# Kernel optimization log

Hardware: AMD Instinct MI355X
Metric: run time of the kernel (lower is better)

The kernel has to match this reference:

```python
import jax, jax.numpy as jnp
import numpy as np

EMBED_DIM = 512
B, N = 8, 2048


def setup_inputs() -> dict:
    key = jax.random.key(0)
    ks = jax.random.split(key, 9)
    d = EMBED_DIM
    s = 1.0 / np.sqrt(d)
    return {
        "x": jax.random.normal(ks[0], (B, N, d), dtype=jnp.float32),
        "Wq": jax.random.uniform(ks[1], (d, d), jnp.float32, -s, s),
        "bq": jax.random.uniform(ks[2], (d,), jnp.float32, -s, s),
        "Wk": jax.random.uniform(ks[3], (d, d), jnp.float32, -s, s),
        "bk": jax.random.uniform(ks[4], (d,), jnp.float32, -s, s),
        "Wv": jax.random.uniform(ks[5], (d, d), jnp.float32, -s, s),
        "bv": jax.random.uniform(ks[6], (d,), jnp.float32, -s, s),
        "Wo": jax.random.uniform(ks[7], (d, d), jnp.float32, -s, s),
        "bo": jax.random.uniform(ks[8], (d,), jnp.float32, -s, s),
    }


def reference(x, Wq, bq, Wk, bk, Wv, bv, Wo, bo):
    d = x.shape[-1]
    scale = d ** (-0.5)
    q = x @ Wq + bq              # [B, N, D]
    k = x @ Wk + bk
    v = x @ Wv + bv
    attn = jnp.einsum('bnd,bmd->bnm', q, k) * scale  # [B, N, N]
    attn = jax.nn.softmax(attn, axis=-1)
    out = jnp.einsum('bnm,bmd->bnd', attn, v)
    return out @ Wo + bo
```

## Files before the change

kernel.cpp:

```cpp
#include <hip/hip_runtime.h>
#include <hip/hip_bf16.h>
#include <hip/hip_fp8.h>
#include <stdint.h>

typedef __bf16 bf16;
typedef __attribute__((ext_vector_type(8))) short short8;
typedef __attribute__((ext_vector_type(4))) float f32x4;
typedef __attribute__((ext_vector_type(4))) bf16 bf16x4;
typedef __attribute__((ext_vector_type(8))) int int8v;
typedef __attribute__((ext_vector_type(4))) int int4v;

#define DIM 512
#define NBATCH 8
#define SEQ 2048

__device__ __forceinline__ void gld_lds16(const void* g, void* l) {
    __builtin_amdgcn_global_load_lds(
        (const __attribute__((address_space(1))) void*)g,
        (__attribute__((address_space(3))) void*)l,
        16, 0, 0);
}

__device__ __forceinline__ unsigned char f32_to_e4m3(float v) {
#if __has_builtin(__builtin_amdgcn_cvt_pk_fp8_f32)
    return (unsigned char)(__builtin_amdgcn_cvt_pk_fp8_f32(v, v, 0, false) & 0xff);
#else
    return __hip_cvt_float_to_fp8(v, __HIP_SATFINITE, __HIP_E4M3);
#endif
}

template <int MODE, int SWIZ>
__global__ __launch_bounds__(256) void gemm_bt(
    const bf16* __restrict__ A, const bf16* __restrict__ Bt,
    void* __restrict__ Cv, const float* __restrict__ bias,
    int N, int K, long long sC, float alpha, int gx)
{
    __shared__ bf16 smem[32768];
    bf16* Asb = smem;
    bf16* Bsb = smem + 16384;

    int bx, by;
    {
        const unsigned g = blockIdx.x;
        const unsigned xcd = g & 7;
        const unsigned t = g >> 3;
        const unsigned per = (gridDim.x >> 3) / (unsigned)gx;
        by = xcd * per + t / (unsigned)gx;
        bx = t % (unsigned)gx;
    }

    const int tid  = threadIdx.x;
    const int lane = tid & 63;
    const int w    = tid >> 6;
    const int wr   = w >> 1;
    const int wc   = w & 1;
    const int lm   = lane & 15;
    const int lk   = lane >> 4;
    const int fs   = lm & 7;
    const int rq   = tid >> 3;
    const int pc   = tid & 7;
    const int scol = ((pc ^ (rq & 7)) * 8);

    const bf16* Ag = A + (size_t)(by * 128) * K;
    const bf16* Bg = Bt + (size_t)(bx * 128) * K;

    f32x4 acc[4][4];
#pragma unroll
    for (int i = 0; i < 4; ++i)
#pragma unroll
        for (int j = 0; j < 4; ++j)
            acc[i][j] = (f32x4){0.f, 0.f, 0.f, 0.f};

    auto stage = [&](int kb, int buf) {
#pragma unroll
        for (int t = 0; t < 4; ++t) {
            const int r = t * 32 + rq;
            gld_lds16(Ag + (size_t)r * K + kb + scol,
                      Asb + buf * 8192 + t * 2048 + tid * 8);
            gld_lds16(Bg + (size_t)r * K + kb + scol,
                      Bsb + buf * 8192 + t * 2048 + tid * 8);
        }
    };
    auto compute = [&](int buf) {
        const bf16* Ab = Asb + buf * 8192;
        const bf16* Bb = Bsb + buf * 8192;
#pragma unroll
        for (int s = 0; s < 2; ++s) {
            const int u = ((s * 4 + lk) ^ fs) * 8;
            short8 fa[4], fb[4];
#pragma unroll
            for (int i = 0; i < 4; ++i)
                fa[i] = *(const short8*)&Ab[(wr * 64 + i * 16 + lm) * 64 + u];
#pragma unroll
            for (int j = 0; j < 4; ++j)
                fb[j] = *(const short8*)&Bb[(wc * 64 + j * 16 + lm) * 64 + u];
#pragma unroll
            for (int i = 0; i < 4; ++i)
#pragma unroll
                for (int j = 0; j < 4; ++j)
                    acc[i][j] = __builtin_amdgcn_mfma_f32_16x16x32_bf16(
                        fa[i], fb[j], acc[i][j], 0, 0, 0);
        }
    };

    stage(0, 0);
    __syncthreads();
    const int E = K >> 6;
#pragma unroll 2
    for (int e = 0; e < E; ++e) {
        if (e + 1 < E) stage((e + 1) << 6, (e + 1) & 1);
        compute(e & 1);
        __syncthreads();
    }

    if (MODE == 2) {
        float* ft = (float*)smem;
        float* outp = (float*)Cv;
#pragma unroll
        for (int h = 0; h < 2; ++h) {
            if (wr == h) {
#pragma unroll
                for (int i = 0; i < 4; ++i)
#pragma unroll
                    for (int j = 0; j < 4; ++j) {
                        const int col = wc * 64 + j * 16 + lm;
                        const float bv = bias[bx * 128 + col];
#pragma unroll
                        for (int r = 0; r < 4; ++r)
                            ft[(i * 16 + lk * 4 + r) * 132 + col] =
                                acc[i][j][r] + bv;
                    }
            }
            __syncthreads();
            const int rr = tid >> 5, cc = (tid & 31) * 4;
#pragma unroll
            for (int p = 0; p < 8; ++p) {
                const int row = p * 8 + rr;
                *(float4*)&outp[(size_t)(by * 128 + h * 64 + row) * N +
                                bx * 128 + cc] = *(const float4*)&ft[row * 132 + cc];
            }
            __syncthreads();
        }
        return;
    }

#pragma unroll
    for (int i = 0; i < 4; ++i)
#pragma unroll
        for (int j = 0; j < 4; ++j) {
            const int col = bx * 128 + wc * 64 + j * 16 + lm;
            const float bv = bias[col];
#pragma unroll
            for (int r = 0; r < 4; ++r)
                acc[i][j][r] += bv;
        }

    const int sub  = (bx * 128) >> 9;
    const int col0 = (bx * 128) & 511;

    if (sub < 2) {
        uint8_t* d8 = (uint8_t*)Cv + (size_t)sub * 8388608;
        uint8_t* t8 = (uint8_t*)smem;
#pragma unroll
        for (int h = 0; h < 2; ++h) {
            if (wr == h) {
#pragma unroll
                for (int i = 0; i < 4; ++i)
#pragma unroll
                    for (int j = 0; j < 4; ++j)
#pragma unroll
                        for (int r = 0; r < 4; ++r)
                            t8[(i * 16 + lk * 4 + r) * 144 + wc * 64 + j * 16 + lm] =
                                f32_to_e4m3(32.0f * acc[i][j][r]);
            }
            __syncthreads();
            const int rr = tid >> 3, cc = (tid & 7) * 16;
#pragma unroll
            for (int p = 0; p < 2; ++p) {
                const int row = p * 32 + rr;
                const uint4 raw = *(const uint4*)&t8[row * 144 + cc];
                *(uint4*)&d8[(size_t)(by * 128 + h * 64 + row) * 512 + col0 + cc] =
                    raw;
            }
            __syncthreads();
        }
    } else {
        bf16* dst = (bf16*)((uint8_t*)Cv + 16777216);
#pragma unroll
        for (int h = 0; h < 2; ++h) {
            if (wr == h) {
#pragma unroll
                for (int i = 0; i < 4; ++i)
#pragma unroll
                    for (int j = 0; j < 4; ++j)
#pragma unroll
                        for (int r = 0; r < 4; ++r)
                            smem[(i * 16 + lk * 4 + r) * 136 + wc * 64 + j * 16 + lm] =
                                (bf16)acc[i][j][r];
            }
            __syncthreads();
            const int rr0 = tid >> 4, cc = (tid & 15) * 8;
#pragma unroll
            for (int p = 0; p < 4; ++p) {
                const int row = p * 16 + rr0;
                const uint4 raw = *(const uint4*)&smem[row * 136 + cc];
                *(uint4*)&dst[(size_t)(by * 128 + h * 64 + row) * 512 + col0 + cc] =
                    raw;
            }
            __syncthreads();
        }
    }
}

template <int MODE>
__global__ __launch_bounds__(256) void gemm_mx(
    const uint8_t* __restrict__ A, const uint8_t* __restrict__ Bt,
    void* __restrict__ Cv, float* __restrict__ rsum,
    int N, int K, long long sA, long long sB, long long sC, float alpha,
    int gx)
{
    __shared__ uint8_t smem[32768];
    uint8_t* As = smem;
    uint8_t* Bs = smem + 16384;

    int bx, by, bz;
    {
        const unsigned g = blockIdx.x;
        bz = g & 7;
        const unsigned r = g >> 3;
        bx = r % (unsigned)gx;
        by = r / (unsigned)gx;
    }

    const int tid  = threadIdx.x;
    const int lane = tid & 63;
    const int w    = tid >> 6;
    const int wr   = w >> 1;
    const int wc   = w & 1;
    const int lm   = lane & 15;
    const int lk   = lane >> 4;
    const int rq   = tid >> 3;
    const int pc   = tid & 7;
    const int ssrc = (pc ^ (rq & 7)) * 16;
    const int ca   = ((2 * lk) ^ (lm & 7)) * 16;
    const int cb   = ((2 * lk + 1) ^ (lm & 7)) * 16;

    const size_t z = bz;
    const uint8_t* Ag = A + z * (size_t)sA + (size_t)(by * 128) * K;
    const uint8_t* Bg = Bt + z * (size_t)sB + (size_t)(bx * 128) * K;

    f32x4 acc[4][4];
#pragma unroll
    for (int i = 0; i < 4; ++i)
#pragma unroll
        for (int j = 0; j < 4; ++j)
            acc[i][j] = (f32x4){0.f, 0.f, 0.f, 0.f};

    for (int kb = 0; kb < K; kb += 128) {
#pragma unroll
        for (int t = 0; t < 4; ++t) {
            const int r = t * 32 + rq;
            gld_lds16(Ag + (size_t)r * K + kb + ssrc, As + t * 4096 + tid * 16);
            gld_lds16(Bg + (size_t)r * K + kb + ssrc, Bs + t * 4096 + tid * 16);
        }
        __syncthreads();

        int8v fa[4];
#pragma unroll
        for (int i = 0; i < 4; ++i) {
            const uint8_t* rp = As + (wr * 64 + i * 16 + lm) * 128;
            const int4v lo = *(const int4v*)(rp + ca);
            const int4v hi = *(const int4v*)(rp + cb);
            fa[i] = (int8v){lo[0], lo[1], lo[2], lo[3], hi[0], hi[1], hi[2], hi[3]};
        }
#pragma unroll
        for (int j = 0; j < 4; ++j) {
            const uint8_t* rp = Bs + (wc * 64 + j * 16 + lm) * 128;
            const int4v lo = *(const int4v*)(rp + ca);
            const int4v hi = *(const int4v*)(rp + cb);
            const int8v fb = (int8v){lo[0], lo[1], lo[2], lo[3],
                                     hi[0], hi[1], hi[2], hi[3]};
#pragma unroll
            for (int i = 0; i < 4; ++i)
                acc[i][j] = __builtin_amdgcn_mfma_scale_f32_16x16x128_f8f6f4(
                    fa[i], fb, acc[i][j], 0, 0, 0, 127, 0, 127);
        }
        __syncthreads();
    }

    const int orow0 = by * 128 + wr * 64;

    if (MODE == 4) {
#pragma unroll
        for (int i = 0; i < 4; ++i) {
            float psum[4] = {0.f, 0.f, 0.f, 0.f};
#pragma unroll
            for (int j = 0; j < 4; ++j)
#pragma unroll
                for (int r = 0; r < 4; ++r) {
                    const float e = __expf(acc[i][j][r] * alpha);
                    acc[i][j][r] = e;
                    psum[r] += e;
                }
#pragma unroll
            for (int m = 1; m < 16; m <<= 1)
#pragma unroll
                for (int r = 0; r < 4; ++r) psum[r] += __shfl_xor(psum[r], m);
            if (lm == 0) {
#pragma unroll
                for (int r = 0; r < 4; ++r)
                    atomicAdd(&rsum[z * SEQ + orow0 + i * 16 + lk * 4 + r],
                              psum[r]);
            }
        }
        uint8_t* dst = (uint8_t*)Cv + z * (size_t)sC;
#pragma unroll
        for (int h = 0; h < 2; ++h) {
            if (wr == h) {
#pragma unroll
                for (int i = 0; i < 4; ++i)
#pragma unroll
                    for (int j = 0; j < 4; ++j)
#pragma unroll
                        for (int r = 0; r < 4; ++r)
                            smem[(i * 16 + lk * 4 + r) * 144 +
                                 wc * 64 + j * 16 + lm] =
                                f32_to_e4m3(acc[i][j][r]);
            }
            __syncthreads();
            const int rr = tid >> 3, cc = (tid & 7) * 16;
#pragma unroll
            for (int p = 0; p < 2; ++p) {
                const int row = p * 32 + rr;
                const uint4 raw = *(const uint4*)&smem[row * 144 + cc];
                *(uint4*)&dst[(size_t)(by * 128 + h * 64 + row) * N +
                              bx * 128 + cc] = raw;
            }
            __syncthreads();
        }
        return;
    }

#pragma unroll
    for (int i = 0; i < 4; ++i) {
        float inv[4];
#pragma unroll
        for (int r = 0; r < 4; ++r)
            inv[r] = 1.0f / (32.0f * rsum[z * SEQ + orow0 + i * 16 + lk * 4 + r]);
#pragma unroll
        for (int j = 0; j < 4; ++j)
#pragma unroll
            for (int r = 0; r < 4; ++r)
                acc[i][j][r] *= inv[r];
    }
    bf16* dst = (bf16*)Cv + z * (size_t)sC;
    bf16* tile = (bf16*)smem;
#pragma unroll
    for (int h = 0; h < 2; ++h) {
        if (wr == h) {
#pragma unroll
            for (int i = 0; i < 4; ++i)
#pragma unroll
                for (int j = 0; j < 4; ++j)
#pragma unroll
                    for (int r = 0; r < 4; ++r)
                        tile[(i * 16 + lk * 4 + r) * 136 + wc * 64 + j * 16 + lm] =
                            (bf16)acc[i][j][r];
        }
        __syncthreads();
        const int rr0 = tid >> 4, cc = (tid & 15) * 8;
#pragma unroll
        for (int p = 0; p < 4; ++p) {
            const int row = p * 16 + rr0;
            const uint4 raw = *(const uint4*)&tile[row * 136 + cc];
            *(uint4*)&dst[(size_t)(by * 128 + h * 64 + row) * N + bx * 128 + cc] =
                raw;
        }
        __syncthreads();
    }
}

__global__ __launch_bounds__(256) void transpose_v(
    const bf16* __restrict__ V, uint8_t* __restrict__ Vt)
{
    __shared__ bf16 tile[64][72];
    const int b = blockIdx.z, tx = blockIdx.x, ty = blockIdx.y;
    const int t0 = threadIdx.x;
#pragma unroll
    for (int it = 0; it < 2; ++it) {
        const int idx = it * 256 + t0;
        const int r = idx >> 3, c0 = (idx & 7) * 8;
        const uint4 raw = *(const uint4*)&V[((size_t)b * SEQ + ty * 64 + r) * 512 +
                                            tx * 64 + c0];
        const bf16* v8 = (const bf16*)&raw;
#pragma unroll
        for (int j = 0; j < 8; ++j) tile[c0 + j][r] = v8[j];
    }
    __syncthreads();
#pragma unroll
    for (int it = 0; it < 2; ++it) {
        const int idx = it * 256 + t0;
        const int o = idx >> 3, i0 = (idx & 7) * 8;
        uint2 pk;
        uint8_t* pb = (uint8_t*)&pk;
#pragma unroll
        for (int j = 0; j < 8; ++j)
            pb[j] = f32_to_e4m3(32.0f * (float)tile[o][i0 + j]);
        *(uint2*)&Vt[((size_t)b * 512 + tx * 64 + o) * SEQ + ty * 64 + i0] = pk;
    }
}

__global__ __launch_bounds__(256) void cvt_f32_bf16(
    const float* __restrict__ x, bf16* __restrict__ o, int n4)
{
    const int i = blockIdx.x * 256 + threadIdx.x;
    if (i >= n4) return;
    const float4 v = ((const float4*)x)[i];
    bf16x4 b;
    b[0] = (bf16)v.x; b[1] = (bf16)v.y; b[2] = (bf16)v.z; b[3] = (bf16)v.w;
    ((bf16x4*)o)[i] = b;
}

__global__ __launch_bounds__(256) void transpose4(
    const float* __restrict__ Wq, const float* __restrict__ Wk,
    const float* __restrict__ Wv, const float* __restrict__ Wo,
    bf16* __restrict__ Wcat, bf16* __restrict__ Wto,
    const float* __restrict__ bq, const float* __restrict__ bk,
    const float* __restrict__ bv, float* __restrict__ bcat,
    float* __restrict__ rowsum)
{
    const int widx = blockIdx.z;
    const int t0 = threadIdx.x;
    if (widx == 4) {
        const int idx = (blockIdx.y * 8 + blockIdx.x) * 256 + t0;
        rowsum[idx] = 0.0f;
        if (idx < 1536)
            bcat[idx] = (idx < 512) ? bq[idx]
                      : (idx < 1024) ? bk[idx - 512] : bv[idx - 1024];
        return;
    }
    __shared__ bf16 tile[64][65];
    const float* W = (widx == 0) ? Wq : (widx == 1) ? Wk : (widx == 2) ? Wv : Wo;
    bf16* dst = (widx < 3) ? (Wcat + (size_t)widx * 512 * 512) : Wto;
    const int tx = blockIdx.x, ty = blockIdx.y;
#pragma unroll
    for (int it = 0; it < 16; ++it) {
        const int e = it * 256 + t0;
        const int r = e >> 6, c = e & 63;
        tile[r][c] = (bf16)W[(size_t)(ty * 64 + r) * 512 + tx * 64 + c];
    }
    __syncthreads();
#pragma unroll
    for (int it = 0; it < 16; ++it) {
        const int e = it * 256 + t0;
        const int o = e >> 6, i = e & 63;
        dst[(size_t)(tx * 64 + o) * 512 + ty * 64 + i] = tile[i][o];
    }
}

extern "C" void kernel_launch(void* const* d_in, const int* in_sizes, int n_in,
                              void* d_out, int out_size, void* d_ws, size_t ws_size,
                              hipStream_t stream)
{
    const float* x  = (const float*)d_in[0];
    const float* Wq = (const float*)d_in[1];
    const float* bq = (const float*)d_in[2];
    const float* Wk = (const float*)d_in[3];
    const float* bk = (const float*)d_in[4];
    const float* Wv = (const float*)d_in[5];
    const float* bv = (const float*)d_in[6];
    const float* Wo = (const float*)d_in[7];
    const float* bo = (const float*)d_in[8];
    float* out = (float*)d_out;

    char* ws = (char*)d_ws;
    bf16*    Xb     = (bf16*)(ws);
    bf16*    Ctx    = (bf16*)(ws);
    bf16*    Wcat   = (bf16*)(ws + 16777216);
    bf16*    Wto    = (bf16*)(ws + 18350080);
    float*   bcat   = (float*)(ws + 18874368);
    float*   rowsum = (float*)(ws + 18880512);
    uint8_t* Q8     = (uint8_t*)(ws + 20971520);
    uint8_t* K8     = (uint8_t*)(ws + 29360128);
    bf16*    V      = (bf16*)(ws + 37748736);
    uint8_t* Vt8    = (uint8_t*)(ws + 54525952);
    uint8_t* S8     = (uint8_t*)(ws + 62914560);

    transpose4<<<dim3(8, 8, 5), 256, 0, stream>>>(
        Wq, Wk, Wv, Wo, Wcat, Wto, bq, bk, bv, bcat, rowsum);
    cvt_f32_bf16<<<8192, 256, 0, stream>>>(x, Xb, 2097152);

    const float scale = 0.044194173824159216f;

    gemm_bt<3, 2><<<1536, 256, 0, stream>>>(
        Xb, Wcat, Q8, bcat, 1536, 512, 0, 1.0f, 12);

    transpose_v<<<dim3(8, 32, 8), 256, 0, stream>>>(V, Vt8);

    gemm_mx<4><<<2048, 256, 0, stream>>>(
        Q8, K8, S8, rowsum, 2048, 512,
        2048LL * 512, 2048LL * 512, 2048LL * 2048, scale / 1024.0f, 16);

    gemm_mx<5><<<512, 256, 0, stream>>>(
        S8, Vt8, Ctx, rowsum, 512, 2048,
        2048LL * 2048, 512LL * 2048, 2048LL * 512, 1.0f, 4);

    gemm_bt<2, 2><<<512, 256, 0, stream>>>(
        Ctx, Wto, out, bo, 512, 512, 0, 1.0f, 4);
}
```

Baseline: 226.2 us.

## Emit V directly as fp8 from the QKV GEMM and transpose bytes only

The QKV projection now writes V in fp8 e4m3 with the same scaling as Q and K instead of bf16, so the V transpose kernel moves bytes and no longer converts. This halves the V write and read traffic and simplifies the transpose. The GEMM kernels also get a minimum-occupancy hint of 3 blocks per CU in their launch bounds, which can force register spilling. With sub==2 the destination offset is 2*8388608, which should land at the V8 offset (ws+37748736 = Q8 base + 16777216), so the layout stays consistent.

```diff
diff --git a/kernel.cpp b/kernel.cpp
--- a/kernel.cpp
+++ b/kernel.cpp
@@ -30,7 +30,7 @@
 }
 
 template <int MODE, int SWIZ>
-__global__ __launch_bounds__(256) void gemm_bt(
+__global__ __launch_bounds__(256, 3) void gemm_bt(
     const bf16* __restrict__ A, const bf16* __restrict__ Bt,
     void* __restrict__ Cv, const float* __restrict__ bias,
     int N, int K, long long sC, float alpha, int gx)
@@ -157,63 +157,35 @@
 
     const int sub  = (bx * 128) >> 9;
     const int col0 = (bx * 128) & 511;
-
-    if (sub < 2) {
-        uint8_t* d8 = (uint8_t*)Cv + (size_t)sub * 8388608;
-        uint8_t* t8 = (uint8_t*)smem;
-#pragma unroll
-        for (int h = 0; h < 2; ++h) {
-            if (wr == h) {
-#pragma unroll
-                for (int i = 0; i < 4; ++i)
-#pragma unroll
-                    for (int j = 0; j < 4; ++j)
-#pragma unroll
-                        for (int r = 0; r < 4; ++r)
-                            t8[(i * 16 + lk * 4 + r) * 144 + wc * 64 + j * 16 + lm] =
-                                f32_to_e4m3(32.0f * acc[i][j][r]);
-            }
-            __syncthreads();
-            const int rr = tid >> 3, cc = (tid & 7) * 16;
-#pragma unroll
-            for (int p = 0; p < 2; ++p) {
-                const int row = p * 32 + rr;
-                const uint4 raw = *(const uint4*)&t8[row * 144 + cc];
-                *(uint4*)&d8[(size_t)(by * 128 + h * 64 + row) * 512 + col0 + cc] =
-                    raw;
-            }
-            __syncthreads();
-        }
-    } else {
-        bf16* dst = (bf16*)((uint8_t*)Cv + 16777216);
-#pragma unroll
-        for (int h = 0; h < 2; ++h) {
-            if (wr == h) {
-#pragma unroll
-                for (int i = 0; i < 4; ++i)
-#pragma unroll
-                    for (int j = 0; j < 4; ++j)
-#pragma unroll
-                        for (int r = 0; r < 4; ++r)
-                            smem[(i * 16 + lk * 4 + r) * 136 + wc * 64 + j * 16 + lm] =
-                                (bf16)acc[i][j][r];
-            }
-            __syncthreads();
-            const int rr0 = tid >> 4, cc = (tid & 15) * 8;
-#pragma unroll
-            for (int p = 0; p < 4; ++p) {
-                const int row = p * 16 + rr0;
-                const uint4 raw = *(const uint4*)&smem[row * 136 + cc];
-                *(uint4*)&dst[(size_t)(by * 128 + h * 64 + row) * 512 + col0 + cc] =
-                    raw;
-            }
-            __syncthreads();
-        }
+    uint8_t* d8 = (uint8_t*)Cv + (size_t)sub * 8388608;
+    uint8_t* t8 = (uint8_t*)smem;
+#pragma unroll
+    for (int h = 0; h < 2; ++h) {
+        if (wr == h) {
+#pragma unroll
+            for (int i = 0; i < 4; ++i)
+#pragma unroll
+                for (int j = 0; j < 4; ++j)
+#pragma unroll
+                    for (int r = 0; r < 4; ++r)
+                        t8[(i * 16 + lk * 4 + r) * 144 + wc * 64 + j * 16 + lm] =
+                            f32_to_e4m3(32.0f * acc[i][j][r]);
+        }
+        __syncthreads();
+        const int rr = tid >> 3, cc = (tid & 7) * 16;
+#pragma unroll
+        for (int p = 0; p < 2; ++p) {
+            const int row = p * 32 + rr;
+            const uint4 raw = *(const uint4*)&t8[row * 144 + cc];
+            *(uint4*)&d8[(size_t)(by * 128 + h * 64 + row) * 512 + col0 + cc] =
+                raw;
+        }
+        __syncthreads();
     }
 }
 
 template <int MODE>
-__global__ __launch_bounds__(256) void gemm_mx(
+__global__ __launch_bounds__(256, 3) void gemm_mx(
     const uint8_t* __restrict__ A, const uint8_t* __restrict__ Bt,
     void* __restrict__ Cv, float* __restrict__ rsum,
     int N, int K, long long sA, long long sB, long long sC, float alpha,
@@ -380,34 +352,22 @@
     }
 }
 
-__global__ __launch_bounds__(256) void transpose_v(
-    const bf16* __restrict__ V, uint8_t* __restrict__ Vt)
-{
-    __shared__ bf16 tile[64][72];
+__global__ __launch_bounds__(256) void transpose_v8(
+    const uint8_t* __restrict__ V, uint8_t* __restrict__ Vt)
+{
+    __shared__ uint8_t tile[64][68];
     const int b = blockIdx.z, tx = blockIdx.x, ty = blockIdx.y;
     const int t0 = threadIdx.x;
-#pragma unroll
-    for (int it = 0; it < 2; ++it) {
-        const int idx = it * 256 + t0;
-        const int r = idx >> 3, c0 = (idx & 7) * 8;
-        const uint4 raw = *(const uint4*)&V[((size_t)b * SEQ + ty * 64 + r) * 512 +
-                                            tx * 64 + c0];
-        const bf16* v8 = (const bf16*)&raw;
-#pragma unroll
-        for (int j = 0; j < 8; ++j) tile[c0 + j][r] = v8[j];
-    }
+    const int r = t0 >> 2, c0 = (t0 & 3) * 16;
+    *(uint4*)&tile[r][c0] =
+        *(const uint4*)&V[((size_t)b * SEQ + ty * 64 + r) * 512 + tx * 64 + c0];
     __syncthreads();
-#pragma unroll
-    for (int it = 0; it < 2; ++it) {
-        const int idx = it * 256 + t0;
-        const int o = idx >> 3, i0 = (idx & 7) * 8;
-        uint2 pk;
-        uint8_t* pb = (uint8_t*)&pk;
-#pragma unroll
-        for (int j = 0; j < 8; ++j)
-            pb[j] = f32_to_e4m3(32.0f * (float)tile[o][i0 + j]);
-        *(uint2*)&Vt[((size_t)b * 512 + tx * 64 + o) * SEQ + ty * 64 + i0] = pk;
-    }
+    const int o = t0 >> 2, i0 = (t0 & 3) * 16;
+    uint4 pk;
+    uint8_t* pb = (uint8_t*)&pk;
+#pragma unroll
+    for (int j = 0; j < 16; ++j) pb[j] = tile[i0 + j][o];
+    *(uint4*)&Vt[((size_t)b * 512 + tx * 64 + o) * SEQ + ty * 64 + i0] = pk;
 }
 
 __global__ __launch_bounds__(256) void cvt_f32_bf16(
@@ -482,7 +442,7 @@
     float*   rowsum = (float*)(ws + 18880512);
     uint8_t* Q8     = (uint8_t*)(ws + 20971520);
     uint8_t* K8     = (uint8_t*)(ws + 29360128);
-    bf16*    V      = (bf16*)(ws + 37748736);
+    uint8_t* V8     = (uint8_t*)(ws + 37748736);
     uint8_t* Vt8    = (uint8_t*)(ws + 54525952);
     uint8_t* S8     = (uint8_t*)(ws + 62914560);
 
@@ -495,7 +455,7 @@
     gemm_bt<3, 2><<<1536, 256, 0, stream>>>(
         Xb, Wcat, Q8, bcat, 1536, 512, 0, 1.0f, 12);
 
-    transpose_v<<<dim3(8, 32, 8), 256, 0, stream>>>(V, Vt8);
+    transpose_v8<<<dim3(8, 32, 8), 256, 0, stream>>>(V8, Vt8);
 
     gemm_mx<4><<<2048, 256, 0, stream>>>(
         Q8, K8, S8, rowsum, 2048, 512,
```

Result: no change. 223.4 us (-1.2%).
